# Performance work log

Hardware: AMD Instinct MI355X
Metric: run time of the kernel (lower is better)

Reference implementation:

```python
import jax, jax.numpy as jnp
import numpy as np

B, NE, NR, D1, D2, L = 64, 40000, 500, 200, 200, 64
BN_EPS = 1e-5


def _batchnorm(x, gamma, beta):
    # training-mode BatchNorm1d: biased batch statistics over axis 0
    mu = jnp.mean(x, axis=0)
    var = jnp.var(x, axis=0)
    return gamma * (x - mu) * jax.lax.rsqrt(var + BN_EPS) + beta


def setup_inputs() -> dict:
    key = jax.random.key(0)
    ks = jax.random.split(key, 10)
    return {
        "e1_idx": jax.random.randint(ks[0], (B,), 0, NE),
        "r_idx": jax.random.randint(ks[1], (B,), 0, NR),
        "E": jax.random.normal(ks[2], (NE, D1), dtype=jnp.float32),
        "R": jax.random.normal(ks[3], (NR, D2), dtype=jnp.float32),
        # W ~ Uniform(-1, 1) as in the torch module
        "W": jax.random.uniform(ks[4], (D2, D1, D1), dtype=jnp.float32, minval=-1.0, maxval=1.0),
        # literals normalized into [0, 1]
        "lits": jax.random.uniform(ks[5], (NE, L), dtype=jnp.float32),
        "c": jax.random.normal(ks[6], (L,), dtype=jnp.float32) * 0.1,
        # variance buffer must be positive
        "var_l": jax.random.uniform(ks[7], (L,), dtype=jnp.float32, minval=0.5, maxval=1.5),
        "nf": jax.random.normal(ks[8], (NR, L), dtype=jnp.float32) * 0.1,
        "bn0_gamma": jnp.ones((D1,), jnp.float32),
        "bn0_beta": jnp.zeros((D1,), jnp.float32),
        "bn1_gamma": jnp.ones((D1,), jnp.float32),
        "bn1_beta": jnp.zeros((D1,), jnp.float32),
    }


def reference(e1_idx, r_idx, E, R, W, lits, c, var_l, nf,
              bn0_gamma, bn0_beta, bn1_gamma, bn1_beta):
    # --- TuckER core ---
    e1 = E[e1_idx]                                   # (B, d1)
    x = _batchnorm(e1, bn0_gamma, bn0_beta)          # (B, d1)
    r = R[r_idx]                                     # (B, d2)
    W_mat = jnp.einsum('bk,kij->bij', r, W)          # (B, d1, d1)
    x = jnp.einsum('bi,bij->bj', x, W_mat)           # (B, d1)
    x = _batchnorm(x, bn1_gamma, bn1_beta)
    score_l = x @ E.T                                # (B, N)

    # --- KBLN numeric-literal branch ---
    n_h = lits[e1_idx]                               # (B, L)
    # broadcast instead of .repeat: (B, 1, L) - (1, N, L) -> (B, N, L)
    n = n_h[:, None, :] - lits[None, :, :]
    phi = jnp.exp(-jnp.square(n - c) / var_l)        # (B, N, L)
    w_nf = nf[r_idx]                                 # (B, L)
    score_n = jnp.einsum('bnl,bl->bn', phi, w_nf)    # (B, N)

    return jax.nn.sigmoid(score_l + score_n)
```

## Files before the change

### kernel.cpp

```cpp
#include <hip/hip_runtime.h>
#include <math.h>

#define BB    64
#define NEC   40000
#define NRC   500
#define D1C   200
#define D2C   200
#define LLC   64
#define BN_EPS 1e-5f
#define LOG2E 1.4426950408889634f

#define WS_XT    0
#define WS_RT    12800
#define WS_TAP   25600
#define WS_WP    29696
#define WS_SL    33792
#define WS_X2BH  33856
#define WS_X2BL  42048
#define WS_Y     50240

typedef short s8v __attribute__((ext_vector_type(8)));
typedef float f4v __attribute__((ext_vector_type(4)));

__device__ __forceinline__ unsigned short bf16_rne(float x) {
  unsigned b = __float_as_uint(x);
  unsigned r = b + 0x7FFFu + ((b >> 16) & 1u);
  return (unsigned short)(r >> 16);
}
__device__ __forceinline__ void split2(float x, unsigned short& h,
                                       unsigned short& l) {
  h = bf16_rne(x);
  float hf = __uint_as_float(((unsigned)h) << 16);
  l = bf16_rne(x - hf);
}

typedef __attribute__((address_space(1))) const void gvoid_t;
typedef __attribute__((address_space(3))) void lvoid_t;
__device__ __forceinline__ void gload_lds16(const float* g, float* l) {
  __builtin_amdgcn_global_load_lds((gvoid_t*)g, (lvoid_t*)l, 16, 0, 0);
}

__global__ __launch_bounds__(256) void prep_kernel(
    const int* __restrict__ e1_idx, const int* __restrict__ r_idx,
    const float* __restrict__ E, const float* __restrict__ R,
    const float* __restrict__ lits, const float* __restrict__ c,
    const float* __restrict__ var_l, const float* __restrict__ nf,
    const float* __restrict__ bn0g, const float* __restrict__ bn0b,
    float* __restrict__ ws) {
  float* xT  = ws + WS_XT;
  float* rT  = ws + WS_RT;
  float* taP = ws + WS_TAP;
  float* wP  = ws + WS_WP;
  float* sl  = ws + WS_SL;
  int tid = threadIdx.x;
  int bid = blockIdx.x;

  if (bid == 0) {
    if (tid < D1C) {
      int j = tid;
      float ev[64];
      float sum = 0.f, sq = 0.f;
#pragma unroll
      for (int b = 0; b < BB; b++) {
        float e = E[e1_idx[b] * D1C + j];
        ev[b] = e;
        sum += e; sq += e * e;
      }
      float mean = sum * (1.f / 64.f);
      float var  = sq  * (1.f / 64.f) - mean * mean;
      float inv  = __builtin_amdgcn_rsqf(var + BN_EPS);
      float g    = bn0g[j] * inv;
      float be   = bn0b[j] - mean * g;
#pragma unroll
      for (int b = 0; b < BB; b++) {
        xT[j * 64 + b] = g * ev[b] + be;
      }
    }
  } else if (bid <= 4) {
    int part = bid - 1;
    int end = part * 3200 + 3200;
    for (int idx = part * 3200 + tid; idx < end; idx += 256) {
      int k = idx >> 6, b = idx & 63;
      rT[idx] = R[r_idx[b] * D2C + k];
    }
  } else if (bid <= 12) {
    int part = bid - 5;
#pragma unroll
    for (int it = 0; it < 2; it++) {
      int idx = part * 512 + it * 256 + tid;
      int b = idx >> 6, l = idx & 63;
      float s = sqrtf(LOG2E / var_l[l]);
      float a = (lits[e1_idx[b] * LLC + l] - c[l]) * s;
      int bp = (b & 15) * 4 + (b >> 4);
      taP[l * 64 + bp] = a + a;
      wP[l * 64 + bp]  = nf[r_idx[b] * LLC + l] * __builtin_amdgcn_exp2f(-a * a);
    }
    if (bid == 5 && tid < LLC) sl[tid] = sqrtf(LOG2E / var_l[tid]);
  } else {
    unsigned* z = (unsigned*)(ws + WS_X2BH);
    for (int i = (bid - 13) * 256 + tid; i < 16384; i += 768) z[i] = 0u;
  }
}

#define S1_STAGE(buf_, s_) do {                                         \
    int gbase_ = kbase + (s_) * 8000;                                   \
    _Pragma("unroll")                                                   \
    for (int r_ = 0; r_ < 4; r_++) {                                    \
      int off_ = r_ * 2048 + w * 256;                                   \
      int gi_ = gbase_ + off_ + lane4;                                  \
      gi_ = gi_ < 7999996 ? gi_ : 7999996;                              \
      gload_lds16(W + gi_, &Wb[buf_][off_]);                            \
    }                                                                   \
  } while (0)

__global__ __launch_bounds__(512) void stage1_kernel(
    const float* __restrict__ W, const float* __restrict__ ws_in,
    float* __restrict__ y) {
  const float* xTg = ws_in + WS_XT;
  const float* rT  = ws_in + WS_RT;
  __shared__ float Wb[2][8192];
  __shared__ float xTl[12800];

  int k = blockIdx.x;
  int tid = threadIdx.x;
  int lane = tid & 63;
  int w = __builtin_amdgcn_readfirstlane(tid >> 6);
  int jc = w & 3, bh = w >> 2;
  int j4 = lane & 15, bq = lane >> 4;
  int j0 = jc * 64 + j4 * 4;
  int b0 = bh * 32 + bq * 8;
  bool jok = j0 < 200;
  int joff = jok ? j0 : 0;
  int kbase = k * 40000;
  int lane4 = lane * 4;

  for (int cc = w; cc < 50; cc += 8) {
    gload_lds16(xTg + cc * 256 + lane4, &xTl[cc * 256]);
  }
  S1_STAGE(0, 0);

  float acc[4][8];
#pragma unroll
  for (int jj = 0; jj < 4; jj++)
#pragma unroll
    for (int bb = 0; bb < 8; bb++) acc[jj][bb] = 0.f;

  for (int s = 0; s < 5; s++) {
    __syncthreads();
    if (s < 4) S1_STAGE((s + 1) & 1, s + 1);
    const float* Ws = Wb[s & 1];
    const float* xrow = xTl + s * 40 * 64 + b0;
#pragma unroll 8
    for (int ri = 0; ri < 40; ri++) {
      float4 wv  = *(const float4*)(Ws + ri * 200 + joff);
      float4 xa  = *(const float4*)(xrow + ri * 64);
      float4 xb2 = *(const float4*)(xrow + ri * 64 + 4);
      float wc[4] = {wv.x, wv.y, wv.z, wv.w};
      float xv[8] = {xa.x, xa.y, xa.z, xa.w, xb2.x, xb2.y, xb2.z, xb2.w};
#pragma unroll
      for (int jj = 0; jj < 4; jj++)
#pragma unroll
        for (int bb = 0; bb < 8; bb++)
          acc[jj][bb] += wc[jj] * xv[bb];
    }
  }

  if (jok) {
    float4 r0 = *(const float4*)(rT + k * 64 + b0);
    float4 r1 = *(const float4*)(rT + k * 64 + b0 + 4);
    float rv[8] = {r0.x, r0.y, r0.z, r0.w, r1.x, r1.y, r1.z, r1.w};
#pragma unroll
    for (int jj = 0; jj < 4; jj++) {
      float* yo = y + ((j0 + jj) * 200 + k) * 64 + b0;
      float4 o0 = make_float4(acc[jj][0] * rv[0], acc[jj][1] * rv[1],
                              acc[jj][2] * rv[2], acc[jj][3] * rv[3]);
      float4 o1 = make_float4(acc[jj][4] * rv[4], acc[jj][5] * rv[5],
                              acc[jj][6] * rv[6], acc[jj][7] * rv[7]);
      *(float4*)(yo) = o0;
      *(float4*)(yo + 4) = o1;
    }
  }
}

__global__ __launch_bounds__(256) void reduce_bn1_kernel(
    const float* __restrict__ y, const float* __restrict__ bn1g,
    const float* __restrict__ bn1b, float* __restrict__ ws) {
  int j = blockIdx.x;
  int tid = threadIdx.x, b = tid & 63, kq = tid >> 6;

  float s = 0.f;
  const float* yp = y + (j * 200 + kq * 50) * 64 + b;
#pragma unroll 10
  for (int k = 0; k < 50; k++) s += yp[k * 64];

  __shared__ float part[256];
  part[tid] = s;
  __syncthreads();
  if (tid < 64) {
    float v = part[tid] + part[64 + tid] + part[128 + tid] + part[192 + tid];
    float sum = v, sq = v * v;
#pragma unroll
    for (int o = 32; o > 0; o >>= 1) {
      sum += __shfl_xor(sum, o, 64);
      sq  += __shfl_xor(sq,  o, 64);
    }
    float mean = sum * (1.f / 64.f);
    float var  = sq  * (1.f / 64.f) - mean * mean;
    float inv  = __builtin_amdgcn_rsqf(var + BN_EPS);
    float g    = bn1g[j] * inv;
    float be   = bn1b[j] - mean * g;
    float xv   = g * v + be;
    unsigned short h, l;
    split2(xv, h, l);
    unsigned short* xh = (unsigned short*)(ws + WS_X2BH);
    unsigned short* xl = (unsigned short*)(ws + WS_X2BL);
    xh[tid * 256 + j] = h;
    xl[tid * 256 + j] = l;
  }
}

__global__ __launch_bounds__(256, 4) void final_kernel(
    const float* __restrict__ E, const float* __restrict__ lits,
    const float* __restrict__ ws, float* __restrict__ out) {
  const float* taP = ws + WS_TAP;
  const float* wP  = ws + WS_WP;
  const float* sl  = ws + WS_SL;
  const unsigned short* x2bh = (const unsigned short*)(ws + WS_X2BH);
  const unsigned short* x2bl = (const unsigned short*)(ws + WS_X2BL);

  __shared__ float SM[9216];
  unsigned short* Ah = (unsigned short*)SM;
  unsigned short* Al = Ah + 4608;
  unsigned short* Bh = Ah + 9216;
  unsigned short* Bl = Ah + 13824;

  int n0 = blockIdx.x * 64;
  int tid = threadIdx.x;
  int lane = tid & 63;
  int w = __builtin_amdgcn_readfirstlane(tid >> 6);
  int ln = lane & 15;
  int quad = lane >> 4;

  f4v acc[4];
#pragma unroll
  for (int t = 0; t < 4; t++) acc[t] = (f4v){0.f, 0.f, 0.f, 0.f};

  for (int q = 0; q < 4; q++) {
    int k0 = q * 64;
    __syncthreads();
#pragma unroll
    for (int it = 0; it < 4; it++) {
      int idx = tid + it * 256;
      int row = idx >> 4, c4 = idx & 15, cc = c4 * 4;
      float4 v = make_float4(0.f, 0.f, 0.f, 0.f);
      if (k0 + cc < 200) v = *(const float4*)(E + (n0 + row) * D1C + k0 + cc);
      unsigned short h0, l0, h1, l1, h2, l2, h3, l3;
      split2(v.x, h0, l0); split2(v.y, h1, l1);
      split2(v.z, h2, l2); split2(v.w, h3, l3);
      *(ushort4*)(Ah + row * 72 + cc) = make_ushort4(h0, h1, h2, h3);
      *(ushort4*)(Al + row * 72 + cc) = make_ushort4(l0, l1, l2, l3);
    }
#pragma unroll
    for (int it = 0; it < 4; it++) {
      int idx = tid + it * 256;
      int row = idx >> 4, c4 = idx & 15;
      *(ushort4*)(Bh + row * 72 + c4 * 4) =
          *(const ushort4*)(x2bh + row * 256 + k0 + c4 * 4);
      *(ushort4*)(Bl + row * 72 + c4 * 4) =
          *(const ushort4*)(x2bl + row * 256 + k0 + c4 * 4);
    }
    __syncthreads();

    const unsigned short* Ab  = Ah + (16 * w + ln) * 72 + quad * 8;
    const unsigned short* Alb = Al + (16 * w + ln) * 72 + quad * 8;
#pragma unroll
    for (int ks = 0; ks < 64; ks += 32) {
      s8v ah = *(const s8v*)(Ab + ks);
      s8v al = *(const s8v*)(Alb + ks);
#pragma unroll
      for (int t = 0; t < 4; t++) {
        s8v bh = *(const s8v*)(Bh + (16 * t + ln) * 72 + quad * 8 + ks);
        s8v bl = *(const s8v*)(Bl + (16 * t + ln) * 72 + quad * 8 + ks);
        acc[t] = __builtin_amdgcn_mfma_f32_16x16x32_bf16(ah, bh, acc[t], 0, 0, 0);
        acc[t] = __builtin_amdgcn_mfma_f32_16x16x32_bf16(al, bh, acc[t], 0, 0, 0);
        acc[t] = __builtin_amdgcn_mfma_f32_16x16x32_bf16(ah, bl, acc[t], 0, 0, 0);
      }
    }
  }

  float* Llds = SM;
  float* TAl  = SM + 4352;
  float* Wl   = SM + 6400;
  int nlb = 16 * w + 4 * quad;

  __syncthreads();
#pragma unroll
  for (int it = 0; it < 4; it++) {
    int idx = tid + it * 256;
    int row = idx >> 4, c4 = idx & 15;
    float4 v = *(const float4*)(lits + (n0 + row) * LLC + c4 * 4);
    int l = c4 * 4;
    Llds[(l + 0) * 68 + row] = v.x * sl[l + 0];
    Llds[(l + 1) * 68 + row] = v.y * sl[l + 1];
    Llds[(l + 2) * 68 + row] = v.z * sl[l + 2];
    Llds[(l + 3) * 68 + row] = v.w * sl[l + 3];
  }

  for (int h = 0; h < 2; h++) {
    __syncthreads();
#pragma unroll
    for (int it = 0; it < 2; it++) {
      int idx = tid + it * 256;
      ((float4*)TAl)[idx] = ((const float4*)(taP + h * 2048))[idx];
      ((float4*)Wl)[idx]  = ((const float4*)(wP  + h * 2048))[idx];
    }
    __syncthreads();
    for (int ll = 0; ll < 32; ll++) {
      float4 Lv = *(const float4*)(Llds + (h * 32 + ll) * 68 + nlb);
      float4 ta = *(const float4*)(TAl + ll * 64 + 4 * ln);
      float4 wv = *(const float4*)(Wl  + ll * 64 + 4 * ln);
      float Lc[4]  = {Lv.x, Lv.y, Lv.z, Lv.w};
      float tac[4] = {ta.x, ta.y, ta.z, ta.w};
      float wvc[4] = {wv.x, wv.y, wv.z, wv.w};
      float n2[4];
#pragma unroll
      for (int r = 0; r < 4; r++) n2[r] = -Lc[r] * Lc[r];
#pragma unroll
      for (int t = 0; t < 4; t++) {
#pragma unroll
        for (int r = 0; r < 4; r++) {
          acc[t][r] += wvc[t] *
              __builtin_amdgcn_exp2f(__builtin_fmaf(tac[t], Lc[r], n2[r]));
        }
      }
    }
  }

#pragma unroll
  for (int t = 0; t < 4; t++) {
    float4 o;
    o.x = __builtin_amdgcn_rcpf(1.f + __builtin_amdgcn_exp2f(-LOG2E * acc[t][0]));
    o.y = __builtin_amdgcn_rcpf(1.f + __builtin_amdgcn_exp2f(-LOG2E * acc[t][1]));
    o.z = __builtin_amdgcn_rcpf(1.f + __builtin_amdgcn_exp2f(-LOG2E * acc[t][2]));
    o.w = __builtin_amdgcn_rcpf(1.f + __builtin_amdgcn_exp2f(-LOG2E * acc[t][3]));
    *(float4*)(out + (size_t)(16 * t + ln) * NEC + n0 + nlb) = o;
  }
}

extern "C" void kernel_launch(void* const* d_in, const int* in_sizes, int n_in,
                              void* d_out, int out_size, void* d_ws, size_t ws_size,
                              hipStream_t stream) {
  (void)in_sizes; (void)n_in; (void)out_size; (void)ws_size;
  const int*   e1    = (const int*)d_in[0];
  const int*   ri    = (const int*)d_in[1];
  const float* E     = (const float*)d_in[2];
  const float* R     = (const float*)d_in[3];
  const float* W     = (const float*)d_in[4];
  const float* lits  = (const float*)d_in[5];
  const float* c     = (const float*)d_in[6];
  const float* var_l = (const float*)d_in[7];
  const float* nf    = (const float*)d_in[8];
  const float* bn0g  = (const float*)d_in[9];
  const float* bn0b  = (const float*)d_in[10];
  const float* bn1g  = (const float*)d_in[11];
  const float* bn1b  = (const float*)d_in[12];
  float* out = (float*)d_out;
  float* ws  = (float*)d_ws;
  float* y   = ws + WS_Y;

  prep_kernel<<<16, 256, 0, stream>>>(e1, ri, E, R, lits, c, var_l, nf,
                                      bn0g, bn0b, ws);
  stage1_kernel<<<200, 512, 0, stream>>>(W, ws, y);
  reduce_bn1_kernel<<<200, 256, 0, stream>>>(y, bn1g, bn1b, ws);
  final_kernel<<<625, 256, 0, stream>>>(E, lits, ws, out);
}
```

Measured before the change: 185.9 us.

## Fold prep kernel into stage1 and reduce kernels, removing one launch

Removes the separate prep kernel. Each stage1 block now computes the BN0-normalized gathered E rows directly into LDS and fetches its own R column. The literal-branch precompute and the zeroing of the bf16 padding move into extra blocks of the reduce kernel, and only the padding columns are zeroed now. This saves one kernel launch and a global round trip for xT and rT, at the cost of redundant BN0 work in all 200 stage1 blocks.

Result: no change. 187.3 us (+0.8%).

```diff
diff --git a/kernel.cpp b/kernel.cpp
--- a/kernel.cpp
+++ b/kernel.cpp
@@ -38,68 +38,6 @@
 typedef __attribute__((address_space(3))) void lvoid_t;
 __device__ __forceinline__ void gload_lds16(const float* g, float* l) {
   __builtin_amdgcn_global_load_lds((gvoid_t*)g, (lvoid_t*)l, 16, 0, 0);
-}
-
-__global__ __launch_bounds__(256) void prep_kernel(
-    const int* __restrict__ e1_idx, const int* __restrict__ r_idx,
-    const float* __restrict__ E, const float* __restrict__ R,
-    const float* __restrict__ lits, const float* __restrict__ c,
-    const float* __restrict__ var_l, const float* __restrict__ nf,
-    const float* __restrict__ bn0g, const float* __restrict__ bn0b,
-    float* __restrict__ ws) {
-  float* xT  = ws + WS_XT;
-  float* rT  = ws + WS_RT;
-  float* taP = ws + WS_TAP;
-  float* wP  = ws + WS_WP;
-  float* sl  = ws + WS_SL;
-  int tid = threadIdx.x;
-  int bid = blockIdx.x;
-
-  if (bid == 0) {
-    if (tid < D1C) {
-      int j = tid;
-      float ev[64];
-      float sum = 0.f, sq = 0.f;
-#pragma unroll
-      for (int b = 0; b < BB; b++) {
-        float e = E[e1_idx[b] * D1C + j];
-        ev[b] = e;
-        sum += e; sq += e * e;
-      }
-      float mean = sum * (1.f / 64.f);
-      float var  = sq  * (1.f / 64.f) - mean * mean;
-      float inv  = __builtin_amdgcn_rsqf(var + BN_EPS);
-      float g    = bn0g[j] * inv;
-      float be   = bn0b[j] - mean * g;
-#pragma unroll
-      for (int b = 0; b < BB; b++) {
-        xT[j * 64 + b] = g * ev[b] + be;
-      }
-    }
-  } else if (bid <= 4) {
-    int part = bid - 1;
-    int end = part * 3200 + 3200;
-    for (int idx = part * 3200 + tid; idx < end; idx += 256) {
-      int k = idx >> 6, b = idx & 63;
-      rT[idx] = R[r_idx[b] * D2C + k];
-    }
-  } else if (bid <= 12) {
-    int part = bid - 5;
-#pragma unroll
-    for (int it = 0; it < 2; it++) {
-      int idx = part * 512 + it * 256 + tid;
-      int b = idx >> 6, l = idx & 63;
-      float s = sqrtf(LOG2E / var_l[l]);
-      float a = (lits[e1_idx[b] * LLC + l] - c[l]) * s;
-      int bp = (b & 15) * 4 + (b >> 4);
-      taP[l * 64 + bp] = a + a;
-      wP[l * 64 + bp]  = nf[r_idx[b] * LLC + l] * __builtin_amdgcn_exp2f(-a * a);
-    }
-    if (bid == 5 && tid < LLC) sl[tid] = sqrtf(LOG2E / var_l[tid]);
-  } else {
-    unsigned* z = (unsigned*)(ws + WS_X2BH);
-    for (int i = (bid - 13) * 256 + tid; i < 16384; i += 768) z[i] = 0u;
-  }
 }
 
 #define S1_STAGE(buf_, s_) do {                                         \
@@ -114,12 +52,13 @@
   } while (0)
 
 __global__ __launch_bounds__(512) void stage1_kernel(
-    const float* __restrict__ W, const float* __restrict__ ws_in,
-    float* __restrict__ y) {
-  const float* xTg = ws_in + WS_XT;
-  const float* rT  = ws_in + WS_RT;
+    const int* __restrict__ e1_idx, const int* __restrict__ r_idx,
+    const float* __restrict__ E, const float* __restrict__ R,
+    const float* __restrict__ bn0g, const float* __restrict__ bn0b,
+    const float* __restrict__ W, float* __restrict__ y) {
   __shared__ float Wb[2][8192];
   __shared__ float xTl[12800];
+  __shared__ float rl[64];
 
   int k = blockIdx.x;
   int tid = threadIdx.x;
@@ -134,10 +73,28 @@
   int kbase = k * 40000;
   int lane4 = lane * 4;
 
-  for (int cc = w; cc < 50; cc += 8) {
-    gload_lds16(xTg + cc * 256 + lane4, &xTl[cc * 256]);
-  }
   S1_STAGE(0, 0);
+
+  if (tid < 64) rl[tid] = R[r_idx[tid] * D2C + k];
+
+  int eb = e1_idx[lane] * D1C;
+#pragma unroll 5
+  for (int t = 0; t < 25; t++) {
+    int j = w + 8 * t;
+    float e = E[eb + j];
+    float sum = e, sq = e * e;
+#pragma unroll
+    for (int o = 32; o > 0; o >>= 1) {
+      sum += __shfl_xor(sum, o, 64);
+      sq  += __shfl_xor(sq,  o, 64);
+    }
+    float mean = sum * (1.f / 64.f);
+    float var  = sq  * (1.f / 64.f) - mean * mean;
+    float inv  = __builtin_amdgcn_rsqf(var + BN_EPS);
+    float g    = bn0g[j] * inv;
+    float be   = bn0b[j] - mean * g;
+    xTl[j * 64 + lane] = g * e + be;
+  }
 
   float acc[4][8];
 #pragma unroll
@@ -166,8 +123,8 @@
   }
 
   if (jok) {
-    float4 r0 = *(const float4*)(rT + k * 64 + b0);
-    float4 r1 = *(const float4*)(rT + k * 64 + b0 + 4);
+    float4 r0 = *(const float4*)(rl + b0);
+    float4 r1 = *(const float4*)(rl + b0 + 4);
     float rv[8] = {r0.x, r0.y, r0.z, r0.w, r1.x, r1.y, r1.z, r1.w};
 #pragma unroll
     for (int jj = 0; jj < 4; jj++) {
@@ -183,39 +140,70 @@
 }
 
 __global__ __launch_bounds__(256) void reduce_bn1_kernel(
-    const float* __restrict__ y, const float* __restrict__ bn1g,
+    const float* __restrict__ y, const float* __restrict__ lits,
+    const float* __restrict__ c, const float* __restrict__ var_l,
+    const float* __restrict__ nf, const int* __restrict__ e1_idx,
+    const int* __restrict__ r_idx, const float* __restrict__ bn1g,
     const float* __restrict__ bn1b, float* __restrict__ ws) {
-  int j = blockIdx.x;
-  int tid = threadIdx.x, b = tid & 63, kq = tid >> 6;
-
-  float s = 0.f;
-  const float* yp = y + (j * 200 + kq * 50) * 64 + b;
+  int bid = blockIdx.x;
+  int tid = threadIdx.x;
+
+  if (bid < 200) {
+    int j = bid;
+    int b = tid & 63, kq = tid >> 6;
+    float s = 0.f;
+    const float* yp = y + (j * 200 + kq * 50) * 64 + b;
 #pragma unroll 10
-  for (int k = 0; k < 50; k++) s += yp[k * 64];
-
-  __shared__ float part[256];
-  part[tid] = s;
-  __syncthreads();
-  if (tid < 64) {
-    float v = part[tid] + part[64 + tid] + part[128 + tid] + part[192 + tid];
-    float sum = v, sq = v * v;
-#pragma unroll
-    for (int o = 32; o > 0; o >>= 1) {
-      sum += __shfl_xor(sum, o, 64);
-      sq  += __shfl_xor(sq,  o, 64);
-    }
-    float mean = sum * (1.f / 64.f);
-    float var  = sq  * (1.f / 64.f) - mean * mean;
-    float inv  = __builtin_amdgcn_rsqf(var + BN_EPS);
-    float g    = bn1g[j] * inv;
-    float be   = bn1b[j] - mean * g;
-    float xv   = g * v + be;
-    unsigned short h, l;
-    split2(xv, h, l);
-    unsigned short* xh = (unsigned short*)(ws + WS_X2BH);
-    unsigned short* xl = (unsigned short*)(ws + WS_X2BL);
-    xh[tid * 256 + j] = h;
-    xl[tid * 256 + j] = l;
+    for (int k = 0; k < 50; k++) s += yp[k * 64];
+
+    __shared__ float part[256];
+    part[tid] = s;
+    __syncthreads();
+    if (tid < 64) {
+      float v = part[tid] + part[64 + tid] + part[128 + tid] + part[192 + tid];
+      float sum = v, sq = v * v;
+#pragma unroll
+      for (int o = 32; o > 0; o >>= 1) {
+        sum += __shfl_xor(sum, o, 64);
+        sq  += __shfl_xor(sq,  o, 64);
+      }
+      float mean = sum * (1.f / 64.f);
+      float var  = sq  * (1.f / 64.f) - mean * mean;
+      float inv  = __builtin_amdgcn_rsqf(var + BN_EPS);
+      float g    = bn1g[j] * inv;
+      float be   = bn1b[j] - mean * g;
+      float xv   = g * v + be;
+      unsigned short h, l;
+      split2(xv, h, l);
+      unsigned short* xh = (unsigned short*)(ws + WS_X2BH);
+      unsigned short* xl = (unsigned short*)(ws + WS_X2BL);
+      xh[tid * 256 + j] = h;
+      xl[tid * 256 + j] = l;
+    }
+  } else if (bid <= 207) {
+    float* taP = ws + WS_TAP;
+    float* wP  = ws + WS_WP;
+    float* sl  = ws + WS_SL;
+    int part = bid - 200;
+#pragma unroll
+    for (int it = 0; it < 2; it++) {
+      int idx = part * 512 + it * 256 + tid;
+      int b = idx >> 6, l = idx & 63;
+      float s = sqrtf(LOG2E / var_l[l]);
+      float a = (lits[e1_idx[b] * LLC + l] - c[l]) * s;
+      int bp = (b & 15) * 4 + (b >> 4);
+      taP[l * 64 + bp] = a + a;
+      wP[l * 64 + bp]  = nf[r_idx[b] * LLC + l] * __builtin_amdgcn_exp2f(-a * a);
+    }
+    if (bid == 200 && tid < LLC) sl[tid] = sqrtf(LOG2E / var_l[tid]);
+  } else {
+    unsigned* z = (unsigned*)(ws + WS_X2BH);
+    for (int idx = tid; idx < 64 * 28 * 2; idx += 256) {
+      int a  = idx >= 1792 ? 1 : 0;
+      int i2 = idx - a * 1792;
+      int r  = i2 / 28, cw = i2 % 28;
+      z[a * 8192 + r * 128 + 100 + cw] = 0u;
+    }
   }
 }
 
@@ -368,9 +356,8 @@
   float* ws  = (float*)d_ws;
   float* y   = ws + WS_Y;
 
-  prep_kernel<<<16, 256, 0, stream>>>(e1, ri, E, R, lits, c, var_l, nf,
-                                      bn0g, bn0b, ws);
-  stage1_kernel<<<200, 512, 0, stream>>>(W, ws, y);
-  reduce_bn1_kernel<<<200, 256, 0, stream>>>(y, bn1g, bn1b, ws);
+  stage1_kernel<<<200, 512, 0, stream>>>(e1, ri, E, R, bn0g, bn0b, W, y);
+  reduce_bn1_kernel<<<209, 256, 0, stream>>>(y, lits, c, var_l, nf,
+                                             e1, ri, bn1g, bn1b, ws);
   final_kernel<<<625, 256, 0, stream>>>(E, lits, ws, out);
 }
```
